# Performance work log

Measured on AMD Instinct MI355X. Metric: run time of the kernel, lower is better.

The kernel has to match this reference:

```python
import jax, jax.numpy as jnp
import numpy as np
import math

B, S, H = 2, 2048, 768
NH, HD = 12, 64  # num_sparse_heads, attention_head_size
VOCAB = 30522


def setup_inputs() -> dict:
    key = jax.random.key(0)
    ks = jax.random.split(key, 6)
    scale = 0.02
    return {
        "hidden_states": jax.random.normal(ks[0], (B, S, H), dtype=jnp.float32),
        "attention_mask": jnp.zeros((B, S), dtype=jnp.float32),
        "input_ids": jax.random.randint(ks[1], (B, S), 0, VOCAB, dtype=jnp.int64) if jax.config.read('jax_enable_x64') else jax.random.randint(ks[1], (B, S), 0, VOCAB, dtype=jnp.int32),
        "ngram": 1,
        "Wq": jax.random.normal(ks[2], (H, H), dtype=jnp.float32) * scale,
        "bq": jnp.zeros((H,), dtype=jnp.float32),
        "Wk": jax.random.normal(ks[3], (H, H), dtype=jnp.float32) * scale,
        "bk": jnp.zeros((H,), dtype=jnp.float32),
    }


def reference(hidden_states, attention_mask, input_ids, ngram, Wq, bq, Wk, bk):
    # Linear projections (torch Linear: x @ W.T + b)
    q = hidden_states @ Wq.T + bq  # [B, S, H]
    k = hidden_states @ Wk.T + bk  # [B, S, H]
    # split heads -> [B, NH, S, HD]
    q = q.reshape(B, S, NH, HD).transpose(0, 2, 1, 3)
    k = k.reshape(B, S, NH, HD).transpose(0, 2, 1, 3)
    # QK^T scores, scale, additive mask over the QUERY axis (mask[:, None, :, None]), ReLU
    scores = jnp.einsum('bhqd,bhkd->bhqk', q, k) / math.sqrt(HD)
    scores = scores + attention_mask[:, None, :, None]
    probs = jax.nn.relu(scores)
    # context_layer = probs.transpose(1, 2) -> [B, S, NH, S]
    return jnp.swapaxes(probs, 1, 2)
```

## Files before the change

kernel.cpp:

```cpp
#include <hip/hip_runtime.h>
#include <hip/hip_bf16.h>
#include <stdint.h>

#define Bb  2
#define Ss  2048
#define Hh  768
#define NHh 12
#define HDd 64

typedef short bf16x8 __attribute__((ext_vector_type(8)));
typedef float f32x4  __attribute__((ext_vector_type(4)));
typedef unsigned short u16x4 __attribute__((ext_vector_type(4)));

__device__ __forceinline__ unsigned short f2bf(float x) {
    union { float f; unsigned int u; } v; v.f = x;
    unsigned int r = v.u + 0x7fffu + ((v.u >> 16) & 1u);
    return (unsigned short)(r >> 16);
}

__device__ __forceinline__ void gl_lds16(const unsigned short* g, unsigned short* l) {
    __builtin_amdgcn_global_load_lds(
        (const __attribute__((address_space(1))) unsigned int*)g,
        (__attribute__((address_space(3))) unsigned int*)l, 16, 0, 0);
}

__global__ __launch_bounds__(256)
void cast_kernel(const float* __restrict__ hs, const float* __restrict__ Wq,
                 const float* __restrict__ Wk,
                 unsigned short* __restrict__ hsb, unsigned short* __restrict__ Wqb,
                 unsigned short* __restrict__ Wkb)
{
    int cid = blockIdx.x * 256 + threadIdx.x;
    const float* src; unsigned short* dst; int base;
    if (cid < 393216)      { src = hs; dst = hsb; base = cid; }
    else if (cid < 466944) { src = Wq; dst = Wqb; base = cid - 393216; }
    else                   { src = Wk; dst = Wkb; base = cid - 466944; }
    float4 a0 = ((const float4*)src)[(size_t)base * 2];
    float4 a1 = ((const float4*)src)[(size_t)base * 2 + 1];
    bf16x8 v;
    v[0] = (short)f2bf(a0.x); v[1] = (short)f2bf(a0.y);
    v[2] = (short)f2bf(a0.z); v[3] = (short)f2bf(a0.w);
    v[4] = (short)f2bf(a1.x); v[5] = (short)f2bf(a1.y);
    v[6] = (short)f2bf(a1.z); v[7] = (short)f2bf(a1.w);
    ((bf16x8*)dst)[base] = v;
}

__global__ __launch_bounds__(256)
void proj_kernel(const unsigned short* __restrict__ hsb,
                 const unsigned short* __restrict__ Wqb,
                 const unsigned short* __restrict__ Wkb,
                 const float* __restrict__ bq, const float* __restrict__ bk,
                 unsigned short* __restrict__ Qb, unsigned short* __restrict__ Kb)
{
    const int zq = blockIdx.z;
    const unsigned short* __restrict__ Wb = zq ? Wkb : Wqb;
    const float* __restrict__ bias = zq ? bk : bq;
    unsigned short* __restrict__ Out = zq ? Kb : Qb;

    const int m0 = blockIdx.x * 128;
    const int n0 = blockIdx.y * 128;

    __shared__ unsigned short As[128 * 64];
    __shared__ unsigned short Bs[128 * 64];

    const int tid  = threadIdx.x;
    const int lane = tid & 63;
    const int w    = tid >> 6;
    const int wm   = (w >> 1) * 64;
    const int wn   = (w & 1) * 64;
    const int lg   = lane >> 4;
    const int l15  = lane & 15;

    f32x4 acc[4][4] = {};

    for (int k0 = 0; k0 < Hh; k0 += 64) {
        #pragma unroll
        for (int i = 0; i < 4; ++i) {
            int cc  = i * 256 + tid;
            int row = cc >> 3, seg = (cc & 7) * 8;
            gl_lds16(hsb + (size_t)(m0 + row) * Hh + k0 + seg, &As[cc * 8]);
            gl_lds16(Wb  + (size_t)(n0 + row) * Hh + k0 + seg, &Bs[cc * 8]);
        }
        __syncthreads();

        #pragma unroll
        for (int kk = 0; kk < 2; ++kk) {
            const int kof = kk * 32 + lg * 8;
            bf16x8 wf[4], hf[4];
            #pragma unroll
            for (int i = 0; i < 4; ++i)
                wf[i] = *(bf16x8*)&Bs[(wm + i * 16 + l15) * 64 + kof];
            #pragma unroll
            for (int j = 0; j < 4; ++j)
                hf[j] = *(bf16x8*)&As[(wn + j * 16 + l15) * 64 + kof];
            #pragma unroll
            for (int i = 0; i < 4; ++i)
                #pragma unroll
                for (int j = 0; j < 4; ++j)
                    acc[i][j] = __builtin_amdgcn_mfma_f32_16x16x32_bf16(
                        wf[i], hf[j], acc[i][j], 0, 0, 0);
        }
        __syncthreads();
    }

    #pragma unroll
    for (int i = 0; i < 4; ++i) {
        const int nb = n0 + wm + i * 16 + lg * 4;
        const float4 bv = *(const float4*)&bias[nb];
        #pragma unroll
        for (int j = 0; j < 4; ++j) {
            const int m = m0 + wn + j * 16 + l15;
            u16x4 o;
            o[0] = f2bf(acc[i][j][0] + bv.x);
            o[1] = f2bf(acc[i][j][1] + bv.y);
            o[2] = f2bf(acc[i][j][2] + bv.z);
            o[3] = f2bf(acc[i][j][3] + bv.w);
            *(u16x4*)&Out[(size_t)m * Hh + nb] = o;
        }
    }
}

__global__ __launch_bounds__(256)
void score_kernel(const unsigned short* __restrict__ Qb,
                  const unsigned short* __restrict__ Kb,
                  const float* __restrict__ mask,
                  float* __restrict__ out)
{
    const int q0 = blockIdx.x * 128;
    const int c0 = blockIdx.y * 128;
    const int bh = blockIdx.z;
    const int b  = bh / NHh, h = bh % NHh;

    const int tid  = threadIdx.x;
    const int lane = tid & 63;
    const int w    = tid >> 6;
    const int wm   = (w >> 1) * 64;
    const int wn   = (w & 1) * 64;
    const int lg   = lane >> 4;
    const int l15  = lane & 15;

    const unsigned short* Qbase = Qb + (size_t)(b * Ss + q0 + wn) * Hh + h * HDd;
    const unsigned short* Kbase = Kb + (size_t)(b * Ss + c0 + wm) * Hh + h * HDd;

    f32x4 acc[4][4] = {};
    #pragma unroll
    for (int kk = 0; kk < 2; ++kk) {
        const int kof = kk * 32 + lg * 8;
        bf16x8 kf[4], qf[4];
        #pragma unroll
        for (int m = 0; m < 4; ++m)
            kf[m] = *(const bf16x8*)&Kbase[(size_t)(m * 16 + l15) * Hh + kof];
        #pragma unroll
        for (int n = 0; n < 4; ++n)
            qf[n] = *(const bf16x8*)&Qbase[(size_t)(n * 16 + l15) * Hh + kof];
        #pragma unroll
        for (int m = 0; m < 4; ++m)
            #pragma unroll
            for (int n = 0; n < 4; ++n)
                acc[m][n] = __builtin_amdgcn_mfma_f32_16x16x32_bf16(
                    kf[m], qf[n], acc[m][n], 0, 0, 0);
    }

    #pragma unroll
    for (int n = 0; n < 4; ++n) {
        const int q = q0 + wn + n * 16 + l15;
        const float mv = mask[b * Ss + q];
        float* orow = out + ((size_t)(b * Ss + q) * NHh + h) * Ss;
        #pragma unroll
        for (int m = 0; m < 4; ++m) {
            const int kb = c0 + wm + m * 16 + lg * 4;
            f32x4 o;
            float v0 = acc[m][n][0] * 0.125f + mv;
            float v1 = acc[m][n][1] * 0.125f + mv;
            float v2 = acc[m][n][2] * 0.125f + mv;
            float v3 = acc[m][n][3] * 0.125f + mv;
            o[0] = v0 > 0.f ? v0 : 0.f;
            o[1] = v1 > 0.f ? v1 : 0.f;
            o[2] = v2 > 0.f ? v2 : 0.f;
            o[3] = v3 > 0.f ? v3 : 0.f;
            *(f32x4*)&orow[kb] = o;
        }
    }
}

extern "C" void kernel_launch(void* const* d_in, const int* in_sizes, int n_in,
                              void* d_out, int out_size, void* d_ws, size_t ws_size,
                              hipStream_t stream) {
    const float* hs   = (const float*)d_in[0];
    const float* mask = (const float*)d_in[1];
    const float* Wq = (const float*)d_in[4];
    const float* bq = (const float*)d_in[5];
    const float* Wk = (const float*)d_in[6];
    const float* bk = (const float*)d_in[7];
    float* out = (float*)d_out;

    unsigned short* Qb  = (unsigned short*)d_ws;
    unsigned short* Kb  = Qb  + 3145728;
    unsigned short* hsb = Kb  + 3145728;
    unsigned short* Wqb = hsb + 3145728;
    unsigned short* Wkb = Wqb + 589824;

    cast_kernel<<<2112, 256, 0, stream>>>(hs, Wq, Wk, hsb, Wqb, Wkb);
    proj_kernel<<<dim3(32, 6, 2), 256, 0, stream>>>(hsb, Wqb, Wkb, bq, bk, Qb, Kb);
    score_kernel<<<dim3(16, 16, 24), 256, 0, stream>>>(Qb, Kb, mask, out);
}
```

Before: 137.7 us.

## Restructure score kernel as per-wave Q-row streaming over double-buffered K tiles

The score kernel now gives each block 64 query rows of one batch-head. Each wave keeps its 16 query fragments in registers and walks all 2048 keys in 64-key tiles, which it loads into a private LDS double buffer using async global-to-LDS copies and an XOR swizzle. This replaces the 6144-block grid, where every block reloaded Q and K tiles from global memory, with 768 persistent-style blocks. The aim is to overlap K fetches with MFMA work and the large fp32 output writes. The trade-offs are lower parallelism (768 blocks, serial loop of 32 tiles), reliance on hand-tuned vmcnt waits without barriers (safe only because each wave owns its buffer), and each output row being written in 64-wide chunks per iteration.

New measurement: 139.8 us. No clear change (+1.5%).

```diff
diff --git a/kernel.cpp b/kernel.cpp
--- a/kernel.cpp
+++ b/kernel.cpp
@@ -126,59 +126,98 @@
                   const float* __restrict__ mask,
                   float* __restrict__ out)
 {
-    const int q0 = blockIdx.x * 128;
-    const int c0 = blockIdx.y * 128;
-    const int bh = blockIdx.z;
-    const int b  = bh / NHh, h = bh % NHh;
+    const int bid = blockIdx.x;
+    const int bh  = bid >> 5;
+    const int qt  = bid & 31;
+    const int b   = bh / NHh, h = bh % NHh;
+
+    __shared__ unsigned short Ks[4][2][4096];
 
     const int tid  = threadIdx.x;
     const int lane = tid & 63;
     const int w    = tid >> 6;
-    const int wm   = (w >> 1) * 64;
-    const int wn   = (w & 1) * 64;
     const int lg   = lane >> 4;
     const int l15  = lane & 15;
-
-    const unsigned short* Qbase = Qb + (size_t)(b * Ss + q0 + wn) * Hh + h * HDd;
-    const unsigned short* Kbase = Kb + (size_t)(b * Ss + c0 + wm) * Hh + h * HDd;
-
-    f32x4 acc[4][4] = {};
+    const int q    = qt * 64 + w * 16 + l15;
+
+    const unsigned short* qrow = Qb + (size_t)(b * Ss + q) * Hh + h * HDd;
+    const bf16x8 qf0 = *(const bf16x8*)&qrow[lg * 8];
+    const bf16x8 qf1 = *(const bf16x8*)&qrow[32 + lg * 8];
+    const float  mv  = mask[b * Ss + q];
+    float* orow = out + ((size_t)(b * Ss + q) * NHh + h) * Ss;
+
+    const unsigned short* kbase = Kb + (size_t)b * Ss * Hh + h * HDd;
+    unsigned short* myk = &Ks[w][0][0];
+
     #pragma unroll
-    for (int kk = 0; kk < 2; ++kk) {
-        const int kof = kk * 32 + lg * 8;
-        bf16x8 kf[4], qf[4];
-        #pragma unroll
-        for (int m = 0; m < 4; ++m)
-            kf[m] = *(const bf16x8*)&Kbase[(size_t)(m * 16 + l15) * Hh + kof];
-        #pragma unroll
-        for (int n = 0; n < 4; ++n)
-            qf[n] = *(const bf16x8*)&Qbase[(size_t)(n * 16 + l15) * Hh + kof];
-        #pragma unroll
-        for (int m = 0; m < 4; ++m)
-            #pragma unroll
-            for (int n = 0; n < 4; ++n)
-                acc[m][n] = __builtin_amdgcn_mfma_f32_16x16x32_bf16(
-                    kf[m], qf[n], acc[m][n], 0, 0, 0);
-    }
-
+    for (int i = 0; i < 8; ++i) {
+        int cc = i * 64 + lane, row = cc >> 3, seg = cc & 7;
+        gl_lds16(kbase + (size_t)row * Hh + ((seg ^ (row & 7)) << 3), myk + cc * 8);
+    }
     #pragma unroll
-    for (int n = 0; n < 4; ++n) {
-        const int q = q0 + wn + n * 16 + l15;
-        const float mv = mask[b * Ss + q];
-        float* orow = out + ((size_t)(b * Ss + q) * NHh + h) * Ss;
+    for (int i = 0; i < 8; ++i) {
+        int cc = i * 64 + lane, row = cc >> 3, seg = cc & 7;
+        gl_lds16(kbase + (size_t)(64 + row) * Hh + ((seg ^ (row & 7)) << 3),
+                 myk + 4096 + cc * 8);
+    }
+    asm volatile("s_waitcnt vmcnt(8)" ::: "memory");
+    __builtin_amdgcn_sched_barrier(0);
+
+    {
+        const unsigned short* src = myk;
         #pragma unroll
         for (int m = 0; m < 4; ++m) {
-            const int kb = c0 + wm + m * 16 + lg * 4;
+            const int row = m * 16 + l15;
+            bf16x8 k0 = *(const bf16x8*)&src[(row << 6) + ((lg ^ (l15 & 7)) << 3)];
+            bf16x8 k1 = *(const bf16x8*)&src[(row << 6) + (((4 + lg) ^ (l15 & 7)) << 3)];
+            f32x4 acc = {};
+            acc = __builtin_amdgcn_mfma_f32_16x16x32_bf16(k0, qf0, acc, 0, 0, 0);
+            acc = __builtin_amdgcn_mfma_f32_16x16x32_bf16(k1, qf1, acc, 0, 0, 0);
             f32x4 o;
-            float v0 = acc[m][n][0] * 0.125f + mv;
-            float v1 = acc[m][n][1] * 0.125f + mv;
-            float v2 = acc[m][n][2] * 0.125f + mv;
-            float v3 = acc[m][n][3] * 0.125f + mv;
+            float v0 = acc[0] * 0.125f + mv;
+            float v1 = acc[1] * 0.125f + mv;
+            float v2 = acc[2] * 0.125f + mv;
+            float v3 = acc[3] * 0.125f + mv;
             o[0] = v0 > 0.f ? v0 : 0.f;
             o[1] = v1 > 0.f ? v1 : 0.f;
             o[2] = v2 > 0.f ? v2 : 0.f;
             o[3] = v3 > 0.f ? v3 : 0.f;
-            *(f32x4*)&orow[kb] = o;
+            *(f32x4*)&orow[m * 16 + lg * 4] = o;
+        }
+    }
+
+    for (int ct = 1; ct < 32; ++ct) {
+        const int buf = ct & 1;
+        const int nct = (ct + 1) & 31;
+        unsigned short* dst = myk + (buf ^ 1) * 4096;
+        #pragma unroll
+        for (int i = 0; i < 8; ++i) {
+            int cc = i * 64 + lane, row = cc >> 3, seg = cc & 7;
+            gl_lds16(kbase + (size_t)(nct * 64 + row) * Hh + ((seg ^ (row & 7)) << 3),
+                     dst + cc * 8);
+        }
+        asm volatile("s_waitcnt vmcnt(12)" ::: "memory");
+        __builtin_amdgcn_sched_barrier(0);
+
+        const unsigned short* src = myk + buf * 4096;
+        #pragma unroll
+        for (int m = 0; m < 4; ++m) {
+            const int row = m * 16 + l15;
+            bf16x8 k0 = *(const bf16x8*)&src[(row << 6) + ((lg ^ (l15 & 7)) << 3)];
+            bf16x8 k1 = *(const bf16x8*)&src[(row << 6) + (((4 + lg) ^ (l15 & 7)) << 3)];
+            f32x4 acc = {};
+            acc = __builtin_amdgcn_mfma_f32_16x16x32_bf16(k0, qf0, acc, 0, 0, 0);
+            acc = __builtin_amdgcn_mfma_f32_16x16x32_bf16(k1, qf1, acc, 0, 0, 0);
+            f32x4 o;
+            float v0 = acc[0] * 0.125f + mv;
+            float v1 = acc[1] * 0.125f + mv;
+            float v2 = acc[2] * 0.125f + mv;
+            float v3 = acc[3] * 0.125f + mv;
+            o[0] = v0 > 0.f ? v0 : 0.f;
+            o[1] = v1 > 0.f ? v1 : 0.f;
+            o[2] = v2 > 0.f ? v2 : 0.f;
+            o[3] = v3 > 0.f ? v3 : 0.f;
+            *(f32x4*)&orow[ct * 64 + m * 16 + lg * 4] = o;
         }
     }
 }
@@ -202,5 +241,5 @@
 
     cast_kernel<<<2112, 256, 0, stream>>>(hs, Wq, Wk, hsb, Wqb, Wkb);
     proj_kernel<<<dim3(32, 6, 2), 256, 0, stream>>>(hsb, Wqb, Wkb, bq, bk, Qb, Kb);
-    score_kernel<<<dim3(16, 16, 24), 256, 0, stream>>>(Qb, Kb, mask, out);
-}
+    score_kernel<<<768, 256, 0, stream>>>(Qb, Kb, mask, out);
+}
```
